# Kernel tuning notes

Measured on AMD Instinct MI355X. Metric: run time of the kernel, lower is better.

Reference implementation:

```python
import jax, jax.numpy as jnp
import numpy as np

N_JOINTS = 24


def rotation_6d_to_matrix(d6):
    """Zhou et al. 6D -> 3x3 rotation. d6: [..., 6] -> [..., 3, 3] (rows b1,b2,b3)."""
    a1, a2 = d6[..., :3], d6[..., 3:]
    b1 = a1 / jnp.linalg.norm(a1, axis=-1, keepdims=True)
    b2 = a2 - jnp.sum(b1 * a2, axis=-1, keepdims=True) * b1
    b2 = b2 / jnp.linalg.norm(b2, axis=-1, keepdims=True)
    b3 = jnp.cross(b1, b2)
    return jnp.stack([b1, b2, b3], axis=-2)


def setup_inputs() -> dict:
    key = jax.random.key(0)
    k1, k2 = jax.random.split(key)
    N = 131072
    angles = jax.random.normal(k1, (N, N_JOINTS, 6), dtype=jnp.float32)
    xyz = jax.random.normal(k2, (1, N_JOINTS, 3), dtype=jnp.float32)
    # simple chain kinematic tree in topological order
    parent_idx = jnp.arange(0, N_JOINTS - 1, dtype=jnp.int64)
    child_idx = jnp.arange(1, N_JOINTS, dtype=jnp.int64)
    return {"angles": angles, "xyz": xyz, "parent_idx": parent_idx, "child_idx": child_idx}


def reference(angles, xyz, parent_idx, child_idx):
    rot = rotation_6d_to_matrix(angles)  # [N, J, 3, 3]
    N = rot.shape[0]
    dtype = rot.dtype
    parent = np.asarray(parent_idx)
    child = np.asarray(child_idx)
    xyz0 = xyz[0]  # [J, 3] reference skeleton
    bottom = jnp.broadcast_to(jnp.array([0.0, 0.0, 0.0, 1.0], dtype=dtype), (N, 1, 4))

    def make_m(r, t):
        # r: [N,3,3], t: [3] -> homogeneous [N,4,4] with translation r @ t
        trans = jnp.einsum('nij,j->ni', r, t)  # [N,3]
        top = jnp.concatenate([r, trans[..., None]], axis=-1)  # [N,3,4]
        return jnp.concatenate([top, bottom], axis=-2)

    M = [None] * N_JOINTS
    M[0] = make_m(rot[:, 0], xyz0[0])
    for p, c in zip(parent, child):
        p, c = int(p), int(c)
        M[c] = M[p] @ make_m(rot[:, c], xyz0[c] - xyz0[p])
    return jnp.stack(M, axis=1)[..., :3, 3]  # [N, J, 3]
```

## Files before the change

### kernel.cpp

```cpp
#include <hip/hip_runtime.h>


#define N_JOINTS 24
#define SAMPLES_PER_BLOCK 32
#define BLOCK_THREADS 128

__global__ __launch_bounds__(BLOCK_THREADS, 4) void fk_kernel(
    const float4* __restrict__ ain,
    const float*  __restrict__ xyz,
    float4* __restrict__ aout)
{
    __shared__ float4 s_buf[SAMPLES_PER_BLOCK * 37];
    __shared__ float  s_t[N_JOINTS * 3];

    const int tid = threadIdx.x;

    if (tid < N_JOINTS) {
        float x = xyz[tid * 3 + 0];
        float y = xyz[tid * 3 + 1];
        float z = xyz[tid * 3 + 2];
        if (tid > 0) {
            x -= xyz[(tid - 1) * 3 + 0];
            y -= xyz[(tid - 1) * 3 + 1];
            z -= xyz[(tid - 1) * 3 + 2];
        }
        s_t[tid * 3 + 0] = x; s_t[tid * 3 + 1] = y; s_t[tid * 3 + 2] = z;
    }

    const size_t in_base = (size_t)blockIdx.x * (SAMPLES_PER_BLOCK * 36);
    #pragma unroll
    for (int it = 0; it < 9; ++it) {
        const int g = tid + BLOCK_THREADS * it;
        const int s = g / 36;
        const int r = g - s * 36;
        s_buf[s * 37 + r] = ain[in_base + g];
    }
    __syncthreads();

    const int s   = tid >> 2;
    const int seg = tid & 3;
    const float4* __restrict__ row = &s_buf[s * 37 + seg * 9];

    float R[9], t[3];
    float o[18];

    #pragma unroll
    for (int p = 0; p < 3; ++p) {
        const float4 v0 = row[p * 3 + 0];
        const float4 v1 = row[p * 3 + 1];
        const float4 v2 = row[p * 3 + 2];
        float d6[12];
        d6[0] = v0.x; d6[1] = v0.y; d6[2]  = v0.z; d6[3]  = v0.w;
        d6[4] = v1.x; d6[5] = v1.y; d6[6]  = v1.z; d6[7]  = v1.w;
        d6[8] = v2.x; d6[9] = v2.y; d6[10] = v2.z; d6[11] = v2.w;

        #pragma unroll
        for (int h = 0; h < 2; ++h) {
            const int jl = p * 2 + h;
            const int j  = seg * 6 + jl;
            const float a1x = d6[h * 6 + 0], a1y = d6[h * 6 + 1], a1z = d6[h * 6 + 2];
            const float a2x = d6[h * 6 + 3], a2y = d6[h * 6 + 4], a2z = d6[h * 6 + 5];

            const float inv1 = rsqrtf(a1x * a1x + a1y * a1y + a1z * a1z);
            const float b1x = a1x * inv1, b1y = a1y * inv1, b1z = a1z * inv1;
            const float dd = b1x * a2x + b1y * a2y + b1z * a2z;
            float b2x = a2x - dd * b1x, b2y = a2y - dd * b1y, b2z = a2z - dd * b1z;
            const float inv2 = rsqrtf(b2x * b2x + b2y * b2y + b2z * b2z);
            b2x *= inv2; b2y *= inv2; b2z *= inv2;
            const float b3x = b1y * b2z - b1z * b2y;
            const float b3y = b1z * b2x - b1x * b2z;
            const float b3z = b1x * b2y - b1y * b2x;
            const float Rj[9] = { b1x, b1y, b1z,  b2x, b2y, b2z,  b3x, b3y, b3z };

            const float tx = s_t[j * 3 + 0], ty = s_t[j * 3 + 1], tz = s_t[j * 3 + 2];
            const float tlx = Rj[0] * tx + Rj[1] * ty + Rj[2] * tz;
            const float tly = Rj[3] * tx + Rj[4] * ty + Rj[5] * tz;
            const float tlz = Rj[6] * tx + Rj[7] * ty + Rj[8] * tz;

            if (jl == 0) {
                #pragma unroll
                for (int k = 0; k < 9; ++k) R[k] = Rj[k];
                t[0] = tlx; t[1] = tly; t[2] = tlz;
            } else {
                t[0] += R[0] * tlx + R[1] * tly + R[2] * tlz;
                t[1] += R[3] * tlx + R[4] * tly + R[5] * tlz;
                t[2] += R[6] * tlx + R[7] * tly + R[8] * tlz;
                float Nn[9];
                #pragma unroll
                for (int r2 = 0; r2 < 3; ++r2)
                    #pragma unroll
                    for (int c = 0; c < 3; ++c)
                        Nn[r2 * 3 + c] = R[r2 * 3 + 0] * Rj[0 * 3 + c]
                                       + R[r2 * 3 + 1] * Rj[1 * 3 + c]
                                       + R[r2 * 3 + 2] * Rj[2 * 3 + c];
                #pragma unroll
                for (int k = 0; k < 9; ++k) R[k] = Nn[k];
            }
            o[jl * 3 + 0] = t[0];
            o[jl * 3 + 1] = t[1];
            o[jl * 3 + 2] = t[2];
        }
    }

    #pragma unroll
    for (int d = 1; d <= 2; d *= 2) {
        float LR[9], Lt[3];
        #pragma unroll
        for (int k = 0; k < 9; ++k) LR[k] = __shfl_up(R[k], (unsigned)d);
        #pragma unroll
        for (int c = 0; c < 3; ++c) Lt[c] = __shfl_up(t[c], (unsigned)d);
        if (seg >= d) {
            float nt0 = Lt[0] + LR[0] * t[0] + LR[1] * t[1] + LR[2] * t[2];
            float nt1 = Lt[1] + LR[3] * t[0] + LR[4] * t[1] + LR[5] * t[2];
            float nt2 = Lt[2] + LR[6] * t[0] + LR[7] * t[1] + LR[8] * t[2];
            float Nn[9];
            #pragma unroll
            for (int r2 = 0; r2 < 3; ++r2)
                #pragma unroll
                for (int c = 0; c < 3; ++c)
                    Nn[r2 * 3 + c] = LR[r2 * 3 + 0] * R[0 * 3 + c]
                                   + LR[r2 * 3 + 1] * R[1 * 3 + c]
                                   + LR[r2 * 3 + 2] * R[2 * 3 + c];
            #pragma unroll
            for (int k = 0; k < 9; ++k) R[k] = Nn[k];
            t[0] = nt0; t[1] = nt1; t[2] = nt2;
        }
    }

    float ER[9], Et[3];
    #pragma unroll
    for (int k = 0; k < 9; ++k) ER[k] = __shfl_up(R[k], 1u);
    #pragma unroll
    for (int c = 0; c < 3; ++c) Et[c] = __shfl_up(t[c], 1u);
    if (seg == 0) {
        ER[0] = 1.f; ER[1] = 0.f; ER[2] = 0.f;
        ER[3] = 0.f; ER[4] = 1.f; ER[5] = 0.f;
        ER[6] = 0.f; ER[7] = 0.f; ER[8] = 1.f;
        Et[0] = 0.f; Et[1] = 0.f; Et[2] = 0.f;
    }

    #pragma unroll
    for (int k = 0; k < 6; ++k) {
        const float ox = o[3 * k + 0], oy = o[3 * k + 1], oz = o[3 * k + 2];
        o[3 * k + 0] = Et[0] + ER[0] * ox + ER[1] * oy + ER[2] * oz;
        o[3 * k + 1] = Et[1] + ER[3] * ox + ER[4] * oy + ER[5] * oz;
        o[3 * k + 2] = Et[2] + ER[6] * ox + ER[7] * oy + ER[8] * oz;
    }

    __syncthreads();
    float2* ob = reinterpret_cast<float2*>(s_buf);
    #pragma unroll
    for (int q = 0; q < 9; ++q) {
        float2 v; v.x = o[2 * q + 0]; v.y = o[2 * q + 1];
        ob[tid * 9 + q] = v;
    }
    __syncthreads();

    const size_t out_base = (size_t)blockIdx.x * (SAMPLES_PER_BLOCK * 18);
    #pragma unroll
    for (int it = 0; it < 4; ++it)
        aout[out_base + tid + BLOCK_THREADS * it] = s_buf[tid + BLOCK_THREADS * it];
    if (tid < 64)
        aout[out_base + 512 + tid] = s_buf[512 + tid];
}

extern "C" void kernel_launch(void* const* d_in, const int* in_sizes, int n_in,
                              void* d_out, int out_size, void* d_ws, size_t ws_size,
                              hipStream_t stream) {
    const float* angles = (const float*)d_in[0];
    const float* xyz    = (const float*)d_in[1];
    float* out = (float*)d_out;

    const int N = in_sizes[0] / (N_JOINTS * 6);
    const int grid = N / SAMPLES_PER_BLOCK;
    fk_kernel<<<grid, BLOCK_THREADS, 0, stream>>>(
        reinterpret_cast<const float4*>(angles), xyz,
        reinterpret_cast<float4*>(out));
}
```

Baseline: 26.59 us.

## Load inputs via direct global-to-LDS loads and make each wave self-contained

Input rows are loaded with global_load_lds straight into shared memory, replacing the register round trip and the padded layout. Each wave now owns its own 16 samples, its own copy of the offset table and its own output staging region. This lets the block-wide barriers be replaced by wave-local waitcnt and sched barriers. The cost is possible LDS bank conflicts from dropping the padding, which was 37, and reliance on per-wave ordering of LDS writes and reads.

```diff
diff --git a/kernel.cpp b/kernel.cpp
--- a/kernel.cpp
+++ b/kernel.cpp
@@ -1,45 +1,53 @@
 #include <hip/hip_runtime.h>
+#include <stdint.h>
 
 
 #define N_JOINTS 24
-#define SAMPLES_PER_BLOCK 32
-#define BLOCK_THREADS 128
+#define SPB 32
+#define BT  128
 
-__global__ __launch_bounds__(BLOCK_THREADS, 4) void fk_kernel(
+#define GLOAD_LDS16(gptr, lptr)                                            \
+  __builtin_amdgcn_global_load_lds(                                        \
+      (const __attribute__((address_space(1))) uint32_t*)(gptr),           \
+      (__attribute__((address_space(3))) uint32_t*)(lptr), 16, 0, 0)
+
+__global__ __launch_bounds__(BT, 4) void fk_kernel(
     const float4* __restrict__ ain,
     const float*  __restrict__ xyz,
     float4* __restrict__ aout)
 {
-    __shared__ float4 s_buf[SAMPLES_PER_BLOCK * 37];
-    __shared__ float  s_t[N_JOINTS * 3];
+    __shared__ float4 s_buf[SPB * 36];
+    __shared__ float  s_t[2][N_JOINTS * 3];
 
-    const int tid = threadIdx.x;
+    const int tid  = threadIdx.x;
+    const int w    = tid >> 6;
+    const int lane = tid & 63;
 
-    if (tid < N_JOINTS) {
-        float x = xyz[tid * 3 + 0];
-        float y = xyz[tid * 3 + 1];
-        float z = xyz[tid * 3 + 2];
-        if (tid > 0) {
-            x -= xyz[(tid - 1) * 3 + 0];
-            y -= xyz[(tid - 1) * 3 + 1];
-            z -= xyz[(tid - 1) * 3 + 2];
+    if (lane < N_JOINTS) {
+        float x = xyz[lane * 3 + 0];
+        float y = xyz[lane * 3 + 1];
+        float z = xyz[lane * 3 + 2];
+        if (lane > 0) {
+            x -= xyz[lane * 3 - 3];
+            y -= xyz[lane * 3 - 2];
+            z -= xyz[lane * 3 - 1];
         }
-        s_t[tid * 3 + 0] = x; s_t[tid * 3 + 1] = y; s_t[tid * 3 + 2] = z;
+        s_t[w][lane * 3 + 0] = x;
+        s_t[w][lane * 3 + 1] = y;
+        s_t[w][lane * 3 + 2] = z;
     }
 
-    const size_t in_base = (size_t)blockIdx.x * (SAMPLES_PER_BLOCK * 36);
+    const size_t gbase = (size_t)blockIdx.x * (SPB * 36) + (size_t)(w * 576 + lane);
     #pragma unroll
     for (int it = 0; it < 9; ++it) {
-        const int g = tid + BLOCK_THREADS * it;
-        const int s = g / 36;
-        const int r = g - s * 36;
-        s_buf[s * 37 + r] = ain[in_base + g];
+        GLOAD_LDS16(ain + gbase + it * 64, &s_buf[w * 576 + it * 64]);
     }
-    __syncthreads();
+    asm volatile("s_waitcnt vmcnt(0) lgkmcnt(0)" ::: "memory");
+    __builtin_amdgcn_sched_barrier(0);
 
     const int s   = tid >> 2;
     const int seg = tid & 3;
-    const float4* __restrict__ row = &s_buf[s * 37 + seg * 9];
+    const float4* __restrict__ row = &s_buf[s * 36 + seg * 9];
 
     float R[9], t[3];
     float o[18];
@@ -72,7 +80,7 @@
             const float b3z = b1x * b2y - b1y * b2x;
             const float Rj[9] = { b1x, b1y, b1z,  b2x, b2y, b2z,  b3x, b3y, b3z };
 
-            const float tx = s_t[j * 3 + 0], ty = s_t[j * 3 + 1], tz = s_t[j * 3 + 2];
+            const float tx = s_t[w][j * 3 + 0], ty = s_t[w][j * 3 + 1], tz = s_t[w][j * 3 + 2];
             const float tlx = Rj[0] * tx + Rj[1] * ty + Rj[2] * tz;
             const float tly = Rj[3] * tx + Rj[4] * ty + Rj[5] * tz;
             const float tlz = Rj[6] * tx + Rj[7] * ty + Rj[8] * tz;
@@ -147,21 +155,19 @@
         o[3 * k + 2] = Et[2] + ER[6] * ox + ER[7] * oy + ER[8] * oz;
     }
 
-    __syncthreads();
     float2* ob = reinterpret_cast<float2*>(s_buf);
     #pragma unroll
     for (int q = 0; q < 9; ++q) {
         float2 v; v.x = o[2 * q + 0]; v.y = o[2 * q + 1];
-        ob[tid * 9 + q] = v;
+        ob[(size_t)w * 1152 + lane * 9 + q] = v;
     }
-    __syncthreads();
 
-    const size_t out_base = (size_t)blockIdx.x * (SAMPLES_PER_BLOCK * 18);
+    const size_t out_base = (size_t)blockIdx.x * (SPB * 18) + (size_t)(w * 288);
     #pragma unroll
     for (int it = 0; it < 4; ++it)
-        aout[out_base + tid + BLOCK_THREADS * it] = s_buf[tid + BLOCK_THREADS * it];
-    if (tid < 64)
-        aout[out_base + 512 + tid] = s_buf[512 + tid];
+        aout[out_base + lane + 64 * it] = s_buf[w * 576 + lane + 64 * it];
+    if (lane < 32)
+        aout[out_base + 256 + lane] = s_buf[w * 576 + 256 + lane];
 }
 
 extern "C" void kernel_launch(void* const* d_in, const int* in_sizes, int n_in,
@@ -172,8 +178,8 @@
     float* out = (float*)d_out;
 
     const int N = in_sizes[0] / (N_JOINTS * 6);
-    const int grid = N / SAMPLES_PER_BLOCK;
-    fk_kernel<<<grid, BLOCK_THREADS, 0, stream>>>(
+    const int grid = N / SPB;
+    fk_kernel<<<grid, BT, 0, stream>>>(
         reinterpret_cast<const float4*>(angles), xyz,
         reinterpret_cast<float4*>(out));
 }
```

Result: slower. 27.27 us (+2.6%).
